# Kernel tuning notes

Measured on AMD Instinct MI355X. Metric: run time of the kernel, lower is better.

## Reference

```python
import jax, jax.numpy as jnp
import numpy as np

N, E, C, NEF, OUT, NUM_ANGLE = 20000, 160000, 32, 1, 128, 7
F = 2 * C + NEF  # edge_fdim = 65


def setup_inputs() -> dict:
    rng = np.random.default_rng(0)
    row = rng.integers(0, N, size=E).astype(np.int32)
    col = rng.integers(0, N, size=E).astype(np.int32)
    # Line-graph incidence pairs (a, b): edge a = (i,j) feeds edge b = (j,k), i.e. col[a] == row[b].
    sort_idx = np.argsort(row, kind='stable')
    row_sorted = row[sort_idx]
    starts = np.searchsorted(row_sorted, col, 'left')
    ends = np.searchsorted(row_sorted, col, 'right')
    counts = ends - starts
    total = int(counts.sum())
    line_src = np.repeat(np.arange(E, dtype=np.int32), counts)
    base = np.repeat(starts, counts)
    within = np.arange(total, dtype=np.int64) - np.repeat(np.cumsum(counts) - counts, counts)
    line_dst = sort_idx[base + within].astype(np.int32)

    key = jax.random.key(0)
    k = jax.random.split(key, 5)
    return {
        'x': jax.random.normal(k[0], (N, C), jnp.float32),
        'edge_attr': jax.random.normal(k[1], (E, NEF), jnp.float32),
        'pos': jax.random.normal(k[2], (N, 3), jnp.float32),
        'W_msg': jax.random.normal(k[3], (OUT, NUM_ANGLE * 2 * F), jnp.float32) * 0.02,
        'b_msg': jax.random.normal(k[4], (OUT,), jnp.float32) * 0.01,
        'edge_index': jnp.asarray(np.stack([row, col]), jnp.int32),
        'line_src': jnp.asarray(line_src),
        'line_dst': jnp.asarray(line_dst),
    }


def reference(x, edge_attr, pos, W_msg, b_msg, edge_index, line_src, line_dst):
    row, col = edge_index[0], edge_index[1]
    num_node = x.shape[0]
    num_edge = row.shape[0]

    # edge_f = [x_row | x_col | edge_attr]  -> [E, F]
    edge_f = jnp.concatenate([x[row], x[col], edge_attr], axis=1)

    # Line graph: edge a=(i,j) feeds edge b=(j,k). Angle at shared node j.
    j = col[line_src]
    u = pos[row[line_src]] - pos[j]  # j -> i
    v = pos[col[line_dst]] - pos[j]  # j -> k
    cos = jnp.sum(u * v, axis=-1) / (
        jnp.linalg.norm(u, axis=-1) * jnp.linalg.norm(v, axis=-1) + 1e-8)
    ang = jnp.arccos(jnp.clip(cos, -1.0 + 1e-7, 1.0 - 1e-7))  # [0, pi]
    abin = jnp.clip((ang / jnp.pi * NUM_ANGLE).astype(jnp.int32), 0, NUM_ANGLE - 1)

    # Per target edge, accumulate neighbor-edge features into (angle bin, in/out slot).
    seg_in = line_dst.astype(jnp.int32) * (NUM_ANGLE * 2) + abin * 2      # incoming a -> b
    seg_out = line_src.astype(jnp.int32) * (NUM_ANGLE * 2) + abin * 2 + 1  # outgoing b seen from a
    vals = jnp.concatenate([edge_f[line_src], edge_f[line_dst]], axis=0)  # [2L, F]
    segs = jnp.concatenate([seg_in, seg_out], axis=0)
    msg = jax.ops.segment_sum(vals, segs, num_segments=num_edge * NUM_ANGLE * 2)
    msg = msg.reshape(num_edge, NUM_ANGLE * 2 * F)  # [E, 910]

    # output = self.message(message)  (Linear with bias)
    edge_hidden = msg @ W_msg.T + b_msg  # [E, OUT]

    # scatter_add into destination nodes (edge_index[1])
    update = jax.ops.segment_sum(edge_hidden, col, num_segments=num_node)  # [N, OUT]
    return update
```

## Files before the change

kernel.cpp:

```cpp
#include <hip/hip_runtime.h>
#include <stdint.h>

#define N_NODES 20000
#define E_EDGES 160000
#define C_DIM 32
#define OUT_DIM 128
#define K_REAL 910
#define KPH 480
#define DEG_CAP 64
#define SEG 1024
#define NSEG 20
#define MT_A (E_EDGES/256)
#define NROWS_B 20224
#define MT_B (NROWS_B/256)
#define PADW ((NROWS_B - N_NODES)*KPH/2)

typedef __attribute__((ext_vector_type(4))) float f32x4;
typedef __attribute__((ext_vector_type(8))) short short8;

__device__ __forceinline__ float bf2f(unsigned short u){
  union { unsigned int i; float f; } v; v.i = ((unsigned int)u) << 16; return v.f;
}
__device__ __forceinline__ unsigned short f2bf(float f){
  union { float f; unsigned int i; } v; v.f = f;
  unsigned int i = v.i;
  unsigned int r = (i + 0x7FFFu + ((i >> 16) & 1u)) >> 16;
  return (unsigned short)r;
}
__device__ __forceinline__ float ldv(const void* p, size_t i, int isbf){
  return isbf ? bf2f(((const unsigned short*)p)[i]) : ((const float*)p)[i];
}
__device__ __forceinline__ int clampi(int v, int hi){
  return ((unsigned)v < (unsigned)hi) ? v : 0;
}

__global__ void k_init(const void* __restrict__ xraw, int* __restrict__ flag,
                       int* __restrict__ cnt, float* __restrict__ out_acc,
                       unsigned short* __restrict__ msgN)
{
  int tid = threadIdx.x;
  if (blockIdx.x == 0){
    __shared__ int s_bad;
    if (tid == 0) s_bad = 0;
    __syncthreads();
    float v = bf2f(((const unsigned short*)xraw)[tid * 2499]);
    if (!(fabsf(v) < 100.0f)) s_bad = 1;
    __syncthreads();
    if (tid == 0) flag[0] = s_bad ? 0 : 1;
  }
  const int Z1 = 2*N_NODES;
  const int Z2 = Z1 + N_NODES*OUT_DIM;
  const int Z3 = Z2 + PADW;
  int* padp = (int*)(msgN + (size_t)N_NODES*KPH);
  for (int i = blockIdx.x*blockDim.x + tid; i < Z3; i += gridDim.x*blockDim.x){
    if (i < Z1) cnt[i] = 0;
    else if (i < Z2) ((int*)out_acc)[i - Z1] = 0;
    else padp[i - Z2] = 0;
  }
}

__global__ void k_prep(const void* __restrict__ pos, const void* __restrict__ W,
                       const int* __restrict__ row, const int* __restrict__ col,
                       float* __restrict__ vecn, int* __restrict__ cnt,
                       unsigned short* __restrict__ Wp,
                       const int* __restrict__ flg)
{
  int isbf = flg[0];
  if (blockIdx.x < MT_A){
    int e = blockIdx.x*256 + threadIdx.x;
    if (e >= E_EDGES) return;
    int r = clampi(row[e], N_NODES), c = clampi(col[e], N_NODES);
    float vx = ldv(pos, (size_t)c*3+0, isbf) - ldv(pos, (size_t)r*3+0, isbf);
    float vy = ldv(pos, (size_t)c*3+1, isbf) - ldv(pos, (size_t)r*3+1, isbf);
    float vz = ldv(pos, (size_t)c*3+2, isbf) - ldv(pos, (size_t)r*3+2, isbf);
    float nn = sqrtf(vx*vx + vy*vy + vz*vz);
    f32x4 vv; vv[0]=vx; vv[1]=vy; vv[2]=vz; vv[3]=nn;
    *(f32x4*)(vecn + (size_t)e*4) = vv;
    atomicAdd(cnt + r, 1);
    atomicAdd(cnt + N_NODES + c, 1);
  } else {
    int i = (blockIdx.x - MT_A)*256 + threadIdx.x;
    if (i >= 2*OUT_DIM*KPH) return;
    int half = i / (OUT_DIM*KPH);
    int rem = i - half*OUT_DIM*KPH;
    int o = rem / KPH, kp = rem - o*KPH;
    float v = 0.f;
    if (kp < 455){
      int t = kp/65, f = kp - t*65;
      v = ldv(W, (size_t)o*K_REAL + (2*t + half)*65 + f, isbf);
    }
    Wp[i] = f2bf(v);
  }
}

__global__ void k_scan1(const int* __restrict__ cnt, int* __restrict__ start2,
                        int* __restrict__ segsum){
  __shared__ int buf[SEG];
  int b = blockIdx.x, arr = b / NSEG, seg = b - arr*NSEG;
  const int* cntp = cnt + (size_t)arr*N_NODES;
  int* startp = start2 + (size_t)arr*(N_NODES+1);
  int tid = threadIdx.x;
  int i = seg*SEG + tid;
  int v = (i < N_NODES) ? cntp[i] : 0;
  buf[tid] = v;
  __syncthreads();
  for (int off = 1; off < SEG; off <<= 1){
    int t = (tid >= off) ? buf[tid-off] : 0;
    __syncthreads();
    buf[tid] += t;
    __syncthreads();
  }
  if (i < N_NODES) startp[i] = buf[tid] - v;
  if (tid == SEG-1) segsum[b] = buf[tid];
}
__global__ void k_scan2(int* segsum){
  int tid = threadIdx.x;
  if (tid < 2){
    int run = 0;
    for (int s = 0; s < NSEG; ++s){
      int v = segsum[tid*NSEG+s]; segsum[tid*NSEG+s] = run; run += v;
    }
  }
}
__global__ void k_scan3(int* __restrict__ start2, int* __restrict__ fill2,
                        const int* __restrict__ segsum){
  int b = blockIdx.x, arr = b / NSEG, seg = b - arr*NSEG;
  int* startp = start2 + (size_t)arr*(N_NODES+1);
  int* fillp  = fill2  + (size_t)arr*N_NODES;
  int tid = threadIdx.x;
  int i = seg*SEG + tid;
  int add = segsum[b];
  if (i < N_NODES){ int s = startp[i] + add; startp[i] = s; fillp[i] = s; }
  if (b == 0 && tid == 0){
    start2[N_NODES] = E_EDGES;
    start2[(N_NODES+1) + N_NODES] = E_EDGES;
  }
}

__global__ void k_scatter(const int* __restrict__ row, const int* __restrict__ col,
                          int* fill2, int* list_row, int* list_col,
                          int* pos_col, int* node_of_pos)
{
  int e = blockIdx.x*blockDim.x + threadIdx.x;
  if (e >= E_EDGES) return;
  int r = clampi(row[e], N_NODES), c = clampi(col[e], N_NODES);
  int p = atomicAdd(fill2 + r, 1);
  if ((unsigned)p < E_EDGES) list_row[p] = e;
  int q = atomicAdd(fill2 + N_NODES + c, 1);
  if ((unsigned)q < E_EDGES){ list_col[q] = e; node_of_pos[q] = c; }
  pos_col[e] = clampi(q, E_EDGES);
}

__global__ __launch_bounds__(256)
void k_msg_node(const void* __restrict__ x, const void* __restrict__ eattr,
                const float* __restrict__ vecn,
                const int* __restrict__ row, const int* __restrict__ col,
                const int* __restrict__ start2,
                const int* __restrict__ list_row, const int* __restrict__ list_col,
                const int* __restrict__ pos_col,
                unsigned short* __restrict__ msg,
                const int* __restrict__ flg, int half)
{
  __shared__ int posT[DEG_CAP];
  __shared__ int othS[DEG_CAP];
  __shared__ float vS[DEG_CAP][4], vT[DEG_CAP][4];
  __shared__ float eS[DEG_CAP];
  __shared__ unsigned short fS[DEG_CAP][64];
  __shared__ float e64[DEG_CAP][8];
  __shared__ unsigned char bins[DEG_CAP][DEG_CAP];

  const float cb1 = 0.9009688679f, cb2 = 0.6234898019f, cb3 = 0.2225209340f;
  const int* start_row = start2;
  const int* start_col = start2 + (N_NODES+1);
  int j = blockIdx.x;
  int tid = threadIdx.x, wv = tid >> 6, lane = tid & 63;
  int clo = start_col[j], chi = start_col[j+1];
  int rlo = start_row[j], rhi = start_row[j+1];
  if (clo < 0) clo = 0; if (chi > E_EDGES) chi = E_EDGES; if (chi < clo) chi = clo;
  if (rlo < 0) rlo = 0; if (rhi > E_EDGES) rhi = E_EDGES; if (rhi < rlo) rhi = rlo;
  int nI = chi - clo, nO = rhi - rlo;
  int nS = half ? nO : nI;
  int nT = half ? nI : nO;
  int slo = half ? rlo : clo;
  int tlo = half ? clo : rlo;
  const int* slist = half ? list_row : list_col;
  const int* tlist = half ? list_col : list_row;
  if (nT == 0) return;
  int isbf = flg[0];

  if (nS <= DEG_CAP && nT <= DEG_CAP){
    int nS4 = (nS + 3) & ~3;
    if (tid < nS){
      int s = clampi(slist[slo+tid], E_EDGES);
      othS[tid] = clampi(half ? col[s] : row[s], N_NODES);
      eS[tid] = ldv(eattr, s, isbf);
      vS[tid][0]=vecn[s*4+0]; vS[tid][1]=vecn[s*4+1];
      vS[tid][2]=vecn[s*4+2]; vS[tid][3]=vecn[s*4+3];
    }
    if (tid < nT){
      int t = clampi(tlist[tlo+tid], E_EDGES);
      posT[tid] = clampi(pos_col[t], E_EDGES);
      vT[tid][0]=vecn[t*4+0]; vT[tid][1]=vecn[t*4+1];
      vT[tid][2]=vecn[t*4+2]; vT[tid][3]=vecn[t*4+3];
    }
    for (int i = tid; i < DEG_CAP*8; i += 256) ((float*)e64)[i] = 0.f;
    { uint4 z = {0,0,0,0};
      ((uint4*)bins)[tid] = z; }
    __syncthreads();
    for (int cidx = tid; cidx < nS*64; cidx += 256){
      int si = cidx >> 6, f = cidx & 63;
      int lo_node = half ? j : othS[si];
      int hi_node = half ? othS[si] : j;
      int src = (f < 32) ? (lo_node*C_DIM + f) : (hi_node*C_DIM + f - 32);
      fS[si][f] = f2bf(ldv(x, (size_t)src, isbf));
    }
    for (int i = tid; i < (nS4 - nS)*64; i += 256)
      fS[nS + (i >> 6)][i & 63] = 0;
    for (int p = tid; p < nS*64; p += 256){
      int si = p >> 6, ti = p & 63;
      if (ti < nT){
        float dot = -(vS[si][0]*vT[ti][0] + vS[si][1]*vT[ti][1] + vS[si][2]*vT[ti][2]);
        float cv = dot / (vS[si][3]*vT[ti][3] + 1e-8f);
        int t = (cv<=cb1)+(cv<=cb2)+(cv<=cb3)+(cv<=-cb3)+(cv<=-cb2)+(cv<=-cb1);
        bins[ti][si] = (unsigned char)t;
        atomicAdd(&e64[ti][t], eS[si]);
      }
    }
    __syncthreads();
    for (int ti = wv; ti < nT; ti += 4){
      float S0=0,S1=0,S2=0,S3=0,S4=0,S5=0,S6=0;
      const unsigned* brow = (const unsigned*)bins[ti];
      for (int s4 = 0; s4 < nS4; s4 += 4){
        unsigned bb = (unsigned)__builtin_amdgcn_readfirstlane((int)brow[s4 >> 2]);
        #pragma unroll
        for (int u = 0; u < 4; ++u){
          int t = (bb >> (8*u)) & 7;
          float val = bf2f(fS[s4 + u][lane]);
          switch(t){
            case 0: S0+=val; break; case 1: S1+=val; break; case 2: S2+=val; break;
            case 3: S3+=val; break; case 4: S4+=val; break; case 5: S5+=val; break;
            default: S6+=val; break;
          }
        }
      }
      unsigned short* mrow = msg + (size_t)posT[ti]*KPH;
      mrow[0*65+lane]=f2bf(S0); mrow[1*65+lane]=f2bf(S1); mrow[2*65+lane]=f2bf(S2);
      mrow[3*65+lane]=f2bf(S3); mrow[4*65+lane]=f2bf(S4); mrow[5*65+lane]=f2bf(S5);
      mrow[6*65+lane]=f2bf(S6);
      if (lane < 7)  mrow[lane*65+64] = f2bf(e64[ti][lane]);
      if (lane < 25) mrow[455+lane] = 0;
    }
  } else {
    for (int ti = wv; ti < nT; ti += 4){
      int te = clampi(tlist[tlo+ti], E_EDGES);
      float tx=vecn[te*4+0], ty=vecn[te*4+1], tz=vecn[te*4+2], tn=vecn[te*4+3];
      float S0=0,S1=0,S2=0,S3=0,S4=0,S5=0,S6=0,S64v=0;
      for (int si = 0; si < nS; ++si){
        int se = clampi(slist[slo+si], E_EDGES);
        float dot = -(vecn[se*4+0]*tx + vecn[se*4+1]*ty + vecn[se*4+2]*tz);
        float cv = dot / (vecn[se*4+3]*tn + 1e-8f);
        int tv = (cv<=cb1)+(cv<=cb2)+(cv<=cb3)+(cv<=-cb3)+(cv<=-cb2)+(cv<=-cb1);
        int t = __builtin_amdgcn_readfirstlane(tv);
        int oth = clampi(half ? col[se] : row[se], N_NODES);
        int lo_node = half ? j : oth;
        int hi_node = half ? oth : j;
        float val = (lane < 32) ? ldv(x, (size_t)lo_node*C_DIM+lane, isbf)
                                : ldv(x, (size_t)hi_node*C_DIM+lane-32, isbf);
        switch(t){
          case 0: S0+=val; break; case 1: S1+=val; break; case 2: S2+=val; break;
          case 3: S3+=val; break; case 4: S4+=val; break; case 5: S5+=val; break;
          default: S6+=val; break;
        }
        S64v += (lane == t) ? ldv(eattr, se, isbf) : 0.f;
      }
      unsigned short* mrow = msg + (size_t)clampi(pos_col[te], E_EDGES)*KPH;
      mrow[0*65+lane]=f2bf(S0); mrow[1*65+lane]=f2bf(S1); mrow[2*65+lane]=f2bf(S2);
      mrow[3*65+lane]=f2bf(S3); mrow[4*65+lane]=f2bf(S4); mrow[5*65+lane]=f2bf(S5);
      mrow[6*65+lane]=f2bf(S6);
      if (lane < 7)  mrow[lane*65+64] = f2bf(S64v);
      if (lane < 25) mrow[455+lane] = 0;
    }
  }
}

__global__ __launch_bounds__(256)
void k_cnt(const float* __restrict__ vecn, const int* __restrict__ row,
           const int* __restrict__ start2, const int* __restrict__ list_col,
           const int* __restrict__ pos_col, uint2* __restrict__ cntb)
{
  int wv = threadIdx.x >> 6, lane = threadIdx.x & 63;
  int b = blockIdx.x*4 + wv;
  if (b >= E_EDGES) return;
  const int* start_col = start2 + (N_NODES+1);
  int j = clampi(row[b], N_NODES);
  int clo = start_col[j], chi = start_col[j+1];
  if (clo < 0) clo = 0; if (chi > E_EDGES) chi = E_EDGES; if (chi < clo) chi = clo;
  int nS = chi - clo;
  const float cb1 = 0.9009688679f, cb2 = 0.6234898019f, cb3 = 0.2225209340f;
  f32x4 vt = *(const f32x4*)(vecn + (size_t)b*4);
  unsigned n0=0,n1=0,n2=0,n3=0,n4=0,n5=0,n6=0;
  for (int base = 0; base < nS; base += 64){
    int ok = (base + lane) < nS;
    int a = ok ? clampi(list_col[clo + base + lane], E_EDGES) : 0;
    f32x4 va = *(const f32x4*)(vecn + (size_t)a*4);
    float dot = -(va[0]*vt[0] + va[1]*vt[1] + va[2]*vt[2]);
    float cv = dot / (va[3]*vt[3] + 1e-8f);
    int t = (cv<=cb1)+(cv<=cb2)+(cv<=cb3)+(cv<=-cb3)+(cv<=-cb2)+(cv<=-cb1);
    if (!ok) t = 7;
    n0 += (unsigned)__popcll(__ballot(t==0));
    n1 += (unsigned)__popcll(__ballot(t==1));
    n2 += (unsigned)__popcll(__ballot(t==2));
    n3 += (unsigned)__popcll(__ballot(t==3));
    n4 += (unsigned)__popcll(__ballot(t==4));
    n5 += (unsigned)__popcll(__ballot(t==5));
    n6 += (unsigned)__popcll(__ballot(t==6));
  }
  if (lane == 0){
    uint2 cw;
    cw.x = min(n0,255u) | (min(n1,255u)<<8) | (min(n2,255u)<<16) | (min(n3,255u)<<24);
    cw.y = min(n4,255u) | (min(n5,255u)<<8) | (min(n6,255u)<<16);
    cntb[clampi(pos_col[b], E_EDGES)] = cw;
  }
}

__global__ __launch_bounds__(256)
void k_msg1(const void* __restrict__ x, const void* __restrict__ eattr,
            const int* __restrict__ col,
            const int* __restrict__ start2,
            const int* __restrict__ list_row, const int* __restrict__ pos_col,
            const uint2* __restrict__ cntb,
            unsigned short* __restrict__ msgN,
            const int* __restrict__ flg)
{
  int wv = threadIdx.x >> 6, lane = threadIdx.x & 63;
  int j = blockIdx.x*4 + wv;
  if (j >= N_NODES) return;
  int isbf = flg[0];
  unsigned short* mrow = msgN + (size_t)j*KPH;
  int rlo = start2[j], rhi = start2[j+1];
  if (rlo < 0) rlo = 0; if (rhi > E_EDGES) rhi = E_EDGES; if (rhi < rlo) rhi = rlo;
  int nT = rhi - rlo;
  if (nT == 0){
    for (int i = lane; i < KPH; i += 64) mrow[i] = 0;
    return;
  }
  float xj = ldv(x, (size_t)j*C_DIM + (lane & 31), isbf);
  float m0=0,m1=0,m2=0,m3=0,m4=0,m5=0,m6=0;
  float me0=0,me1=0,me2=0,me3=0,me4=0,me5=0,me6=0;

  for (int tb = 0; tb < nT; tb += 64){
    int nn = nT - tb; if (nn > 64) nn = 64;
    int ok = lane < nn;
    int te = ok ? clampi(list_row[rlo + tb + lane], E_EDGES) : 0;
    int pp = clampi(pos_col[te], E_EDGES);
    uint2 cw = cntb[pp];
    int oL = clampi(col[te], N_NODES);
    float eL = ok ? ldv(eattr, te, isbf) : 0.f;
    unsigned cxL = ok ? cw.x : 0u;
    unsigned cyL = ok ? cw.y : 0u;

    for (int u = 0; u < nn; u += 8){
      float v[8], ea[8];
      unsigned cxa[8], cya[8];
      #pragma unroll
      for (int q = 0; q < 8; ++q){
        int ti = u + q;
        int o = __shfl(oL, ti);
        unsigned cx = (unsigned)__shfl((int)cxL, ti);
        unsigned cy = (unsigned)__shfl((int)cyL, ti);
        float eb = __shfl(eL, ti);
        if (ti < nn){
          v[q] = (lane < 32) ? xj : ldv(x, (size_t)o*C_DIM + lane - 32, isbf);
          cxa[q] = cx; cya[q] = cy; ea[q] = eb;
        } else {
          v[q] = 0.f; cxa[q] = 0u; cya[q] = 0u; ea[q] = 0.f;
        }
      }
      #pragma unroll
      for (int q = 0; q < 8; ++q){
        float n0=(float)(cxa[q]&255u),  n1=(float)((cxa[q]>>8)&255u),
              n2=(float)((cxa[q]>>16)&255u), n3=(float)(cxa[q]>>24),
              n4=(float)(cya[q]&255u),  n5=(float)((cya[q]>>8)&255u),
              n6=(float)((cya[q]>>16)&255u);
        m0+=n0*v[q]; m1+=n1*v[q]; m2+=n2*v[q]; m3+=n3*v[q];
        m4+=n4*v[q]; m5+=n5*v[q]; m6+=n6*v[q];
        me0+=n0*ea[q]; me1+=n1*ea[q]; me2+=n2*ea[q]; me3+=n3*ea[q];
        me4+=n4*ea[q]; me5+=n5*ea[q]; me6+=n6*ea[q];
      }
    }
  }

  mrow[0*65+lane]=f2bf(m0); mrow[1*65+lane]=f2bf(m1); mrow[2*65+lane]=f2bf(m2);
  mrow[3*65+lane]=f2bf(m3); mrow[4*65+lane]=f2bf(m4); mrow[5*65+lane]=f2bf(m5);
  mrow[6*65+lane]=f2bf(m6);
  if (lane < 7){
    float me = (lane==0)?me0:(lane==1)?me1:(lane==2)?me2:(lane==3)?me3
             : (lane==4)?me4:(lane==5)?me5:me6;
    mrow[lane*65+64] = f2bf(me);
  }
  if (lane < 25) mrow[455+lane] = 0;
}

__global__ __launch_bounds__(256)
void k_gemm(const unsigned short* __restrict__ A,
            const unsigned short* __restrict__ Wp,
            const void* __restrict__ bias,
            const int* __restrict__ flg,
            const int* __restrict__ node_of_pos,
            float* __restrict__ out_acc, int addbias, int ident, int mtiles)
{
  __shared__ union {
    unsigned short Bs[64*512];
    float seg[256][66];
  } sh;
  __shared__ int nids[256];

  int tid = threadIdx.x;
  int w = tid >> 6, lane = tid & 63;
  int lrow = lane & 15, q = lane >> 4;

  int lin = blockIdx.x;
  const int FULLG = (mtiles & ~7) * 2;
  int mt, ch;
  if (lin < FULLG){
    mt = (lin >> 4)*8 + (lin & 7);
    ch = (lin >> 3) & 1;
  } else {
    int r2 = lin - FULLG;
    mt = (mtiles & ~7) + (r2 >> 1);
    ch = r2 & 1;
  }
  int m0 = mt * 256;

  nids[tid] = ident ? ((m0 + tid < N_NODES) ? m0 + tid : N_NODES-1)
                    : clampi(node_of_pos[m0 + tid], N_NODES);

  const unsigned short* abase = A + (size_t)(m0 + w*64 + lrow)*KPH + q*8;
  short8 apf[3][4];
  #pragma unroll
  for (int d = 0; d < 3; ++d)
    #pragma unroll
    for (int rf = 0; rf < 4; ++rf)
      apf[d][rf] = *(const short8*)(abase + (size_t)rf*16*KPH + d*32);

  #pragma unroll
  for (int i = 0; i < 15; ++i){
    int idx = tid + i*256;
    int rr = idx / 60, cc = idx - rr*60;
    const uint4* gq = (const uint4*)(Wp + (size_t)(ch*64 + rr)*KPH + cc*8);
    *(uint4*)(sh.Bs + rr*512 + ((cc ^ (rr & 7))*8)) = *gq;
  }
  __syncthreads();

  f32x4 acc[4][4];
  #pragma unroll
  for (int rf = 0; rf < 4; ++rf)
    #pragma unroll
    for (int nf = 0; nf < 4; ++nf) acc[rf][nf] = (f32x4)0.f;

  #pragma unroll
  for (int k0i = 0; k0i < 15; ++k0i){
    int cur = k0i % 3;
    int c = k0i*4 + q;
    #pragma unroll
    for (int nf = 0; nf < 4; ++nf){
      int rb = nf*16 + lrow;
      short8 bfr = *(const short8*)(sh.Bs + rb*512 + ((c ^ (rb & 7))*8));
      #pragma unroll
      for (int rf = 0; rf < 4; ++rf)
        acc[rf][nf] = __builtin_amdgcn_mfma_f32_16x16x32_bf16(apf[cur][rf], bfr, acc[rf][nf], 0, 0, 0);
    }
    if (k0i + 3 < 15){
      #pragma unroll
      for (int rf = 0; rf < 4; ++rf)
        apf[cur][rf] = *(const short8*)(abase + (size_t)rf*16*KPH + (k0i+3)*32);
    }
  }

  int isbf = flg[0];
  float bvs[4];
  #pragma unroll
  for (int nf = 0; nf < 4; ++nf)
    bvs[nf] = addbias ? ldv(bias, ch*64 + nf*16 + lrow, isbf) : 0.f;

  __syncthreads();
  #pragma unroll
  for (int rf = 0; rf < 4; ++rf)
    #pragma unroll
    for (int r = 0; r < 4; ++r){
      int m = w*64 + rf*16 + q*4 + r;
      #pragma unroll
      for (int nf = 0; nf < 4; ++nf)
        sh.seg[m][nf*16 + lrow] = acc[rf][nf][r] + bvs[nf];
    }
  __syncthreads();
  {
    int o = tid & 63, g = tid >> 6;
    int base = g*64;
    float s = 0.f;
    int curn = nids[base];
    for (int r = 0; r < 64; ++r){
      int m = base + r;
      int nid = nids[m];
      if (nid != curn){
        atomicAdd(out_acc + (size_t)curn*OUT_DIM + ch*64 + o, s);
        s = 0.f; curn = nid;
      }
      s += sh.seg[m][o];
    }
    atomicAdd(out_acc + (size_t)curn*OUT_DIM + ch*64 + o, s);
  }
}

__global__ void k_out(const float* __restrict__ acc, void* __restrict__ outp,
                      const int* __restrict__ flg){
  int i = blockIdx.x*blockDim.x + threadIdx.x;
  if (i >= N_NODES*OUT_DIM) return;
  if (flg[0]) ((unsigned short*)outp)[i] = f2bf(acc[i]);
  else        ((float*)outp)[i] = acc[i];
}

extern "C" void kernel_launch(void* const* d_in, const int* in_sizes, int n_in,
                              void* d_out, int out_size, void* d_ws, size_t ws_size,
                              hipStream_t stream)
{
  const void* x     = d_in[0];
  const void* eattr = d_in[1];
  const void* pos   = d_in[2];
  const void* W     = d_in[3];
  const void* bmsg  = d_in[4];
  const int* eidx = (const int*)d_in[5];
  const int* row = eidx;
  const int* col = eidx + E_EDGES;

  char* ws = (char*)d_ws;
  size_t off = 0;
  auto alloc = [&](size_t b){ size_t o = off; off += (b + 255) & ~(size_t)255; return o; };

  int* dflag        = (int*)(ws + alloc(256));
  float* vecn       = (float*)(ws + alloc((size_t)E_EDGES*16));
  int* cnt          = (int*)(ws + alloc((size_t)2*N_NODES*4));
  int* start2       = (int*)(ws + alloc((size_t)2*(N_NODES+1)*4));
  int* fill2        = (int*)(ws + alloc((size_t)2*N_NODES*4));
  int* segsum       = (int*)(ws + alloc((size_t)2*NSEG*4));
  int* list_row     = (int*)(ws + alloc((size_t)E_EDGES*4));
  int* list_col     = (int*)(ws + alloc((size_t)E_EDGES*4));
  int* pos_col      = (int*)(ws + alloc((size_t)E_EDGES*4));
  int* node_of_pos  = (int*)(ws + alloc((size_t)E_EDGES*4));
  unsigned short* Wp = (unsigned short*)(ws + alloc((size_t)2*OUT_DIM*KPH*2));
  float* out_acc    = (float*)(ws + alloc((size_t)N_NODES*OUT_DIM*4));
  uint2* cntb       = (uint2*)(ws + alloc((size_t)E_EDGES*8));
  unsigned short* msgN = (unsigned short*)(ws + alloc((size_t)NROWS_B*KPH*2));
  unsigned short* msg  = (unsigned short*)(ws + alloc((size_t)E_EDGES*KPH*2));
  (void)off;

  unsigned short* Wp_in  = Wp;
  unsigned short* Wp_out = Wp + (size_t)OUT_DIM*KPH;

  k_init<<<2048, 256, 0, stream>>>(x, dflag, cnt, out_acc, msgN);
  k_prep<<<MT_A + 480, 256, 0, stream>>>(pos, W, row, col, vecn, cnt, Wp, dflag);
  k_scan1<<<2*NSEG, SEG, 0, stream>>>(cnt, start2, segsum);
  k_scan2<<<1, 64, 0, stream>>>(segsum);
  k_scan3<<<2*NSEG, SEG, 0, stream>>>(start2, fill2, segsum);
  k_scatter<<<(E_EDGES+255)/256, 256, 0, stream>>>(row, col, fill2,
                                                   list_row, list_col, pos_col, node_of_pos);

  k_msg_node<<<N_NODES, 256, 0, stream>>>(x, eattr, vecn, row, col, start2,
                                          list_row, list_col, pos_col, msg, dflag, 0);
  k_cnt<<<(E_EDGES+3)/4, 256, 0, stream>>>(vecn, row, start2, list_col, pos_col, cntb);
  k_msg1<<<(N_NODES+3)/4, 256, 0, stream>>>(x, eattr, col, start2,
                                            list_row, pos_col, cntb, msgN, dflag);
  k_gemm<<<dim3(2*MT_A), 256, 0, stream>>>(msg, Wp_in, bmsg, dflag,
                                           node_of_pos, out_acc, 1, 0, MT_A);
  k_gemm<<<dim3(2*MT_B), 256, 0, stream>>>(msgN, Wp_out, bmsg, dflag,
                                           node_of_pos, out_acc, 0, 1, MT_B);

  k_out<<<(N_NODES*OUT_DIM+255)/256, 256, 0, stream>>>(out_acc, d_out, dflag);
}
```

Measured before the change: 342.9 us.

## Fuse angle-bin counting into message kernel and align msg row layout

Removes the separate k_cnt kernel. Per-target angle-bin counts are now computed inside k_msg_node, from the bins already in shared memory (ballot/popcount) or from counters kept in the fallback loop. This avoids recomputing the angles and re-reading vecn and list_col. The msg row layout also changes from 65-wide angle slots to 64-wide feature blocks followed by 7 edge-attr entries, so the stores are aligned, and the weight packing is updated to match. The risk is that in the shared-memory path the count only covers lanes below nS, which is correct only when nS is at most 64, the DEG_CAP bound.

```diff
diff --git a/kernel.cpp b/kernel.cpp
--- a/kernel.cpp
+++ b/kernel.cpp
@@ -85,9 +85,12 @@
     int rem = i - half*OUT_DIM*KPH;
     int o = rem / KPH, kp = rem - o*KPH;
     float v = 0.f;
-    if (kp < 455){
-      int t = kp/65, f = kp - t*65;
+    if (kp < 448){
+      int t = kp >> 6, f = kp & 63;
       v = ldv(W, (size_t)o*K_REAL + (2*t + half)*65 + f, isbf);
+    } else if (kp < 455){
+      int t = kp - 448;
+      v = ldv(W, (size_t)o*K_REAL + (2*t + half)*65 + 64, isbf);
     }
     Wp[i] = f2bf(v);
   }
@@ -159,6 +162,7 @@
                 const int* __restrict__ list_row, const int* __restrict__ list_col,
                 const int* __restrict__ pos_col,
                 unsigned short* __restrict__ msg,
+                uint2* __restrict__ cntb,
                 const int* __restrict__ flg, int half)
 {
   __shared__ int posT[DEG_CAP];
@@ -244,17 +248,32 @@
         }
       }
       unsigned short* mrow = msg + (size_t)posT[ti]*KPH;
-      mrow[0*65+lane]=f2bf(S0); mrow[1*65+lane]=f2bf(S1); mrow[2*65+lane]=f2bf(S2);
-      mrow[3*65+lane]=f2bf(S3); mrow[4*65+lane]=f2bf(S4); mrow[5*65+lane]=f2bf(S5);
-      mrow[6*65+lane]=f2bf(S6);
-      if (lane < 7)  mrow[lane*65+64] = f2bf(e64[ti][lane]);
+      mrow[0*64+lane]=f2bf(S0); mrow[1*64+lane]=f2bf(S1); mrow[2*64+lane]=f2bf(S2);
+      mrow[3*64+lane]=f2bf(S3); mrow[4*64+lane]=f2bf(S4); mrow[5*64+lane]=f2bf(S5);
+      mrow[6*64+lane]=f2bf(S6);
+      if (lane < 7)  mrow[448+lane] = f2bf(e64[ti][lane]);
       if (lane < 25) mrow[455+lane] = 0;
+      int myb = (lane < nS) ? (int)bins[ti][lane] : 7;
+      unsigned n0 = (unsigned)__popcll(__ballot(myb==0));
+      unsigned n1 = (unsigned)__popcll(__ballot(myb==1));
+      unsigned n2 = (unsigned)__popcll(__ballot(myb==2));
+      unsigned n3 = (unsigned)__popcll(__ballot(myb==3));
+      unsigned n4 = (unsigned)__popcll(__ballot(myb==4));
+      unsigned n5 = (unsigned)__popcll(__ballot(myb==5));
+      unsigned n6 = (unsigned)__popcll(__ballot(myb==6));
+      if (lane == 0){
+        uint2 cw;
+        cw.x = n0 | (n1<<8) | (n2<<16) | (n3<<24);
+        cw.y = n4 | (n5<<8) | (n6<<16);
+        cntb[posT[ti]] = cw;
+      }
     }
   } else {
     for (int ti = wv; ti < nT; ti += 4){
       int te = clampi(tlist[tlo+ti], E_EDGES);
       float tx=vecn[te*4+0], ty=vecn[te*4+1], tz=vecn[te*4+2], tn=vecn[te*4+3];
       float S0=0,S1=0,S2=0,S3=0,S4=0,S5=0,S6=0,S64v=0;
+      int n0=0,n1=0,n2=0,n3=0,n4=0,n5=0,n6=0;
       for (int si = 0; si < nS; ++si){
         int se = clampi(slist[slo+si], E_EDGES);
         float dot = -(vecn[se*4+0]*tx + vecn[se*4+1]*ty + vecn[se*4+2]*tz);
@@ -267,59 +286,28 @@
         float val = (lane < 32) ? ldv(x, (size_t)lo_node*C_DIM+lane, isbf)
                                 : ldv(x, (size_t)hi_node*C_DIM+lane-32, isbf);
         switch(t){
-          case 0: S0+=val; break; case 1: S1+=val; break; case 2: S2+=val; break;
-          case 3: S3+=val; break; case 4: S4+=val; break; case 5: S5+=val; break;
-          default: S6+=val; break;
+          case 0: S0+=val; n0++; break; case 1: S1+=val; n1++; break;
+          case 2: S2+=val; n2++; break; case 3: S3+=val; n3++; break;
+          case 4: S4+=val; n4++; break; case 5: S5+=val; n5++; break;
+          default: S6+=val; n6++; break;
         }
         S64v += (lane == t) ? ldv(eattr, se, isbf) : 0.f;
       }
       unsigned short* mrow = msg + (size_t)clampi(pos_col[te], E_EDGES)*KPH;
-      mrow[0*65+lane]=f2bf(S0); mrow[1*65+lane]=f2bf(S1); mrow[2*65+lane]=f2bf(S2);
-      mrow[3*65+lane]=f2bf(S3); mrow[4*65+lane]=f2bf(S4); mrow[5*65+lane]=f2bf(S5);
-      mrow[6*65+lane]=f2bf(S6);
-      if (lane < 7)  mrow[lane*65+64] = f2bf(S64v);
+      mrow[0*64+lane]=f2bf(S0); mrow[1*64+lane]=f2bf(S1); mrow[2*64+lane]=f2bf(S2);
+      mrow[3*64+lane]=f2bf(S3); mrow[4*64+lane]=f2bf(S4); mrow[5*64+lane]=f2bf(S5);
+      mrow[6*64+lane]=f2bf(S6);
+      if (lane < 7)  mrow[448+lane] = f2bf(S64v);
       if (lane < 25) mrow[455+lane] = 0;
-    }
-  }
-}
-
-__global__ __launch_bounds__(256)
-void k_cnt(const float* __restrict__ vecn, const int* __restrict__ row,
-           const int* __restrict__ start2, const int* __restrict__ list_col,
-           const int* __restrict__ pos_col, uint2* __restrict__ cntb)
-{
-  int wv = threadIdx.x >> 6, lane = threadIdx.x & 63;
-  int b = blockIdx.x*4 + wv;
-  if (b >= E_EDGES) return;
-  const int* start_col = start2 + (N_NODES+1);
-  int j = clampi(row[b], N_NODES);
-  int clo = start_col[j], chi = start_col[j+1];
-  if (clo < 0) clo = 0; if (chi > E_EDGES) chi = E_EDGES; if (chi < clo) chi = clo;
-  int nS = chi - clo;
-  const float cb1 = 0.9009688679f, cb2 = 0.6234898019f, cb3 = 0.2225209340f;
-  f32x4 vt = *(const f32x4*)(vecn + (size_t)b*4);
-  unsigned n0=0,n1=0,n2=0,n3=0,n4=0,n5=0,n6=0;
-  for (int base = 0; base < nS; base += 64){
-    int ok = (base + lane) < nS;
-    int a = ok ? clampi(list_col[clo + base + lane], E_EDGES) : 0;
-    f32x4 va = *(const f32x4*)(vecn + (size_t)a*4);
-    float dot = -(va[0]*vt[0] + va[1]*vt[1] + va[2]*vt[2]);
-    float cv = dot / (va[3]*vt[3] + 1e-8f);
-    int t = (cv<=cb1)+(cv<=cb2)+(cv<=cb3)+(cv<=-cb3)+(cv<=-cb2)+(cv<=-cb1);
-    if (!ok) t = 7;
-    n0 += (unsigned)__popcll(__ballot(t==0));
-    n1 += (unsigned)__popcll(__ballot(t==1));
-    n2 += (unsigned)__popcll(__ballot(t==2));
-    n3 += (unsigned)__popcll(__ballot(t==3));
-    n4 += (unsigned)__popcll(__ballot(t==4));
-    n5 += (unsigned)__popcll(__ballot(t==5));
-    n6 += (unsigned)__popcll(__ballot(t==6));
-  }
-  if (lane == 0){
-    uint2 cw;
-    cw.x = min(n0,255u) | (min(n1,255u)<<8) | (min(n2,255u)<<16) | (min(n3,255u)<<24);
-    cw.y = min(n4,255u) | (min(n5,255u)<<8) | (min(n6,255u)<<16);
-    cntb[clampi(pos_col[b], E_EDGES)] = cw;
+      if (lane == 0){
+        uint2 cw;
+        cw.x = (unsigned)min(n0,255) | ((unsigned)min(n1,255)<<8)
+             | ((unsigned)min(n2,255)<<16) | ((unsigned)min(n3,255)<<24);
+        cw.y = (unsigned)min(n4,255) | ((unsigned)min(n5,255)<<8)
+             | ((unsigned)min(n6,255)<<16);
+        cntb[clampi(pos_col[te], E_EDGES)] = cw;
+      }
+    }
   }
 }
 
@@ -390,13 +378,13 @@
     }
   }
 
-  mrow[0*65+lane]=f2bf(m0); mrow[1*65+lane]=f2bf(m1); mrow[2*65+lane]=f2bf(m2);
-  mrow[3*65+lane]=f2bf(m3); mrow[4*65+lane]=f2bf(m4); mrow[5*65+lane]=f2bf(m5);
-  mrow[6*65+lane]=f2bf(m6);
+  mrow[0*64+lane]=f2bf(m0); mrow[1*64+lane]=f2bf(m1); mrow[2*64+lane]=f2bf(m2);
+  mrow[3*64+lane]=f2bf(m3); mrow[4*64+lane]=f2bf(m4); mrow[5*64+lane]=f2bf(m5);
+  mrow[6*64+lane]=f2bf(m6);
   if (lane < 7){
     float me = (lane==0)?me0:(lane==1)?me1:(lane==2)?me2:(lane==3)?me3
              : (lane==4)?me4:(lane==5)?me5:me6;
-    mrow[lane*65+64] = f2bf(me);
+    mrow[448+lane] = f2bf(me);
   }
   if (lane < 25) mrow[455+lane] = 0;
 }
@@ -564,16 +552,13 @@
   k_scan3<<<2*NSEG, SEG, 0, stream>>>(start2, fill2, segsum);
   k_scatter<<<(E_EDGES+255)/256, 256, 0, stream>>>(row, col, fill2,
                                                    list_row, list_col, pos_col, node_of_pos);
-
   k_msg_node<<<N_NODES, 256, 0, stream>>>(x, eattr, vecn, row, col, start2,
-                                          list_row, list_col, pos_col, msg, dflag, 0);
-  k_cnt<<<(E_EDGES+3)/4, 256, 0, stream>>>(vecn, row, start2, list_col, pos_col, cntb);
+                                          list_row, list_col, pos_col, msg, cntb, dflag, 0);
   k_msg1<<<(N_NODES+3)/4, 256, 0, stream>>>(x, eattr, col, start2,
                                             list_row, pos_col, cntb, msgN, dflag);
   k_gemm<<<dim3(2*MT_A), 256, 0, stream>>>(msg, Wp_in, bmsg, dflag,
                                            node_of_pos, out_acc, 1, 0, MT_A);
   k_gemm<<<dim3(2*MT_B), 256, 0, stream>>>(msgN, Wp_out, bmsg, dflag,
                                            node_of_pos, out_acc, 0, 1, MT_B);
-
   k_out<<<(N_NODES*OUT_DIM+255)/256, 256, 0, stream>>>(out_acc, d_out, dflag);
 }
```

Result: faster. 310.1 us (-9.6%).
